# Kernel tuning notes

Hardware: AMD Instinct MI355X
Metric: run time of the kernel (lower is better)

## Reference

```python
import jax, jax.numpy as jnp
import numpy as np

TEMP = 5.0  # temperature_init
# All C(4,2)=6 keep-2-of-4 patterns for 2:4 semi-structured sparsity
PATTERNS = jnp.array([[1,1,0,0],[1,0,1,0],[1,0,0,1],[0,1,1,0],[0,1,0,1],[0,0,1,1]], dtype=jnp.float32)


def masked_linear(x, w, b, alpha, ids):
    # x: [N, I], w: [O, I], alpha: [A, O, I//4, 6], ids: [N]
    A, O, G, P = alpha.shape
    probs = jax.nn.softmax(alpha / TEMP, axis=-1)            # [A, O, G, 6]
    mask = jnp.einsum('aogp,pk->aogk', probs, PATTERNS)      # [A, O, G, 4]
    wm = w[None, :, :] * mask.reshape(A, O, G * 4)           # [A, O, I] per-agent masked weight
    y = jnp.einsum('ni,aoi->nao', x, wm)                     # dense per-agent GEMM
    y = jnp.take_along_axis(y, ids[:, None, None], axis=1)[:, 0, :]
    return y + b


def gru_cell(x, h, w_ih, w_hh, b_ih, b_hh):
    gi = x @ w_ih.T + b_ih
    gh = h @ w_hh.T + b_hh
    i_r, i_z, i_n = jnp.split(gi, 3, axis=-1)
    h_r, h_z, h_n = jnp.split(gh, 3, axis=-1)
    r = jax.nn.sigmoid(i_r + h_r)
    z = jax.nn.sigmoid(i_z + h_z)
    n = jnp.tanh(i_n + r * h_n)
    return (1.0 - z) * n + z * h


def setup_inputs() -> dict:
    key = jax.random.key(0)
    ks = jax.random.split(key, 20)
    B, A, E, H, NA = 1024, 8, 64, 512, 16
    s = 0.05
    d = {}
    d['inputs'] = jax.random.normal(ks[0], (B, A, E), jnp.float32)
    d['hidden_state'] = jax.random.normal(ks[1], (B, A, H), jnp.float32)
    d['agent_ids'] = jax.random.randint(ks[2], (B, A), 0, A, jnp.int32)
    d['fc1_w'] = jax.random.normal(ks[3], (H, E), jnp.float32) * s
    d['fc1_b'] = jax.random.normal(ks[4], (H,), jnp.float32) * s
    d['fc1_alpha'] = jax.random.normal(ks[5], (A, H, E // 4, 6), jnp.float32)
    d['gru_w_ih'] = jax.random.normal(ks[6], (3 * H, H), jnp.float32) * s
    d['gru_w_hh'] = jax.random.normal(ks[7], (3 * H, H), jnp.float32) * s
    d['gru_b_ih'] = jax.random.normal(ks[8], (3 * H,), jnp.float32) * s
    d['gru_b_hh'] = jax.random.normal(ks[9], (3 * H,), jnp.float32) * s
    d['fc2_w'] = jax.random.normal(ks[10], (H, H), jnp.float32) * s
    d['fc2_b'] = jax.random.normal(ks[11], (H,), jnp.float32) * s
    d['fc2_alpha'] = jax.random.normal(ks[12], (A, H, H // 4, 6), jnp.float32)
    d['fc3_w'] = jax.random.normal(ks[13], (H, H), jnp.float32) * s
    d['fc3_b'] = jax.random.normal(ks[14], (H,), jnp.float32) * s
    d['fc3_alpha'] = jax.random.normal(ks[15], (A, H, H // 4, 6), jnp.float32)
    d['fc4_w'] = jax.random.normal(ks[16], (NA, H), jnp.float32) * s
    d['fc4_b'] = jax.random.normal(ks[17], (NA,), jnp.float32) * s
    d['fc4_alpha'] = jax.random.normal(ks[18], (A, NA, H // 4, 6), jnp.float32)
    return d


def reference(inputs, hidden_state, agent_ids,
              fc1_w, fc1_b, fc1_alpha,
              gru_w_ih, gru_w_hh, gru_b_ih, gru_b_hh,
              fc2_w, fc2_b, fc2_alpha,
              fc3_w, fc3_b, fc3_alpha,
              fc4_w, fc4_b, fc4_alpha):
    b, a, e = inputs.shape
    H = hidden_state.shape[-1]
    x = inputs.reshape(-1, e)
    ids = agent_ids.reshape(-1)
    x = jax.nn.relu(masked_linear(x, fc1_w, fc1_b, fc1_alpha, ids))
    h = gru_cell(x, hidden_state.reshape(-1, H), gru_w_ih, gru_w_hh, gru_b_ih, gru_b_hh)
    q = jax.nn.relu(masked_linear(h, fc2_w, fc2_b, fc2_alpha, ids))
    q = jax.nn.relu(masked_linear(q, fc3_w, fc3_b, fc3_alpha, ids))
    q = masked_linear(q, fc4_w, fc4_b, fc4_alpha, ids)
    return q.reshape(b, a, -1), h.reshape(b, a, -1)
```

## Files before the change

### kernel.cpp

```cpp
#include <hip/hip_runtime.h>
#include <hip/hip_bf16.h>

typedef unsigned short ushort_t;
typedef __bf16 bf16x8 __attribute__((ext_vector_type(8)));
typedef unsigned short us8 __attribute__((ext_vector_type(8)));
typedef float f32x4 __attribute__((ext_vector_type(4)));

#define NPAD 8704
#define SENT (1 << 20)

__device__ __forceinline__ ushort_t f2b(float f) {
    union { float f; unsigned int u; } v; v.f = f;
    unsigned int u = v.u;
    unsigned int r = (u + 0x7FFFu + ((u >> 16) & 1u)) >> 16;
    return (ushort_t)r;
}
__device__ __forceinline__ float sigmoidf_(float x) {
    return 1.f / (1.f + __expf(-x));
}

__global__ void fill_kernel(float* out, long long n, float val) {
    long long i = (long long)blockIdx.x * blockDim.x + threadIdx.x;
    if (i < n) out[i] = val;
}

#define PACKSZ(O, K) ((long long)((O) >= 64 ? (O) >> 6 : 1) * ((K) >> 5) * 2048)

__global__ void sort_kernel(const int* __restrict__ ids, int N,
                            int* __restrict__ perm, int* __restrict__ seg,
                            int4* __restrict__ ttab, int* __restrict__ tcount) {
    __shared__ int hist[16][8];
    __shared__ int wbase[16][8];
    __shared__ int atot[8];
    __shared__ int abase[8];
    int tid = threadIdx.x, wave = tid >> 6, lane = tid & 63;
    int base = wave * 512;
    unsigned long long lt = (lane == 63) ? 0x7fffffffffffffffull
                                         : ((1ull << lane) - 1ull);
    int myid[8], rank[8];
    int run[8] = {0, 0, 0, 0, 0, 0, 0, 0};
    #pragma unroll
    for (int i = 0; i < 8; i++) myid[i] = ids[base + i * 64 + lane] & 7;
    #pragma unroll
    for (int i = 0; i < 8; i++) {
        int a = myid[i];
        int r = 0;
        #pragma unroll
        for (int a2 = 0; a2 < 8; a2++) {
            unsigned long long m = __ballot(a == a2);
            if (a2 == a) r = run[a2] + __popcll(m & lt);
            run[a2] += __popcll(m);
        }
        rank[i] = r;
    }
    if (lane == 0) {
        #pragma unroll
        for (int a = 0; a < 8; a++) hist[wave][a] = run[a];
    }
    __syncthreads();
    if (tid < 8) {
        int a = tid, s = 0;
        for (int w = 0; w < 16; w++) { wbase[w][a] = s; s += hist[w][a]; }
        atot[a] = s;
    }
    __syncthreads();
    if (tid == 0) {
        int s = 0;
        for (int a = 0; a < 8; a++) {
            abase[a] = s; seg[a] = s;
            s += (atot[a] + 63) & ~63;
        }
        seg[8] = s;
        int T = 0;
        for (int a = 0; a < 8; a++) {
            int e = abase[a] + atot[a];
            int pe = abase[a] + ((atot[a] + 63) & ~63);
            for (int m = abase[a]; m < pe; m += 64) {
                int z = e < m + 64 ? e : m + 64;
                ttab[T++] = make_int4(a, m, z, 0);
            }
        }
        *tcount = T;
    }
    __syncthreads();
    #pragma unroll
    for (int i = 0; i < 8; i++) {
        int a = myid[i];
        perm[abase[a] + wbase[wave][a] + rank[i]] = base + i * 64 + lane;
    }
    for (int a = 0; a < 8; a++) {
        int e = abase[a] + atot[a];
        int pe = abase[a] + ((atot[a] + 63) & ~63);
        for (int p2 = e + tid; p2 < pe; p2 += 1024) perm[p2] = SENT;
    }
    int Pend = abase[7] + ((atot[7] + 63) & ~63);
    for (int p2 = Pend + tid; p2 < NPAD; p2 += 1024) perm[p2] = SENT;
}

__device__ __forceinline__ void maskw_item(const float* __restrict__ alpha,
                                           const float* __restrict__ w,
                                           ushort_t* __restrict__ wm,
                                           long long idx, int O, int G, int dup) {
    int g = (int)(idx % G);
    long long t2 = idx / G;
    int o = (int)(t2 % O);
    int a = (int)(t2 / O);
    const float* al = alpha + idx * 6;
    float p[6];
    float mx = -1e30f;
    #pragma unroll
    for (int i = 0; i < 6; i++) { p[i] = al[i] * 0.2f; mx = fmaxf(mx, p[i]); }
    float s = 0.f;
    #pragma unroll
    for (int i = 0; i < 6; i++) { p[i] = __expf(p[i] - mx); s += p[i]; }
    float inv = 1.f / s;
    #pragma unroll
    for (int i = 0; i < 6; i++) p[i] *= inv;
    float mk[4] = { p[0] + p[1] + p[2], p[0] + p[3] + p[4],
                    p[1] + p[3] + p[5], p[2] + p[4] + p[5] };
    int K = G * 4;
    const float* wr = w + (long long)o * K + g * 4;
    ushort_t* base = wm + (long long)a * PACKSZ(O, K);
    int k0 = g * 4;
    int c = o >> 6, su = (o >> 4) & 3, n = o & 15;
    int kk = k0 >> 5, q = (k0 >> 3) & 3, e0 = k0 & 7;
    long long off = (((long long)(c * (K >> 5) + kk) * 4 + su) * 64 + (q * 16 + n)) * 8 + e0;
    #pragma unroll
    for (int t = 0; t < 4; t++) {
        ushort_t v = f2b(wr[t] * mk[t]);
        base[off + t] = v;
        if (dup) {
            base[off + t + 512] = v;
            base[off + t + 1024] = v;
            base[off + t + 1536] = v;
        }
    }
}

__device__ __forceinline__ void canon_gather_packed(const float* __restrict__ src,
                                                    ushort_t* __restrict__ dst,
                                                    const int* __restrict__ perm,
                                                    int ld, long long i) {
    int l = (int)(i & 63);
    int tt = (int)(i >> 6);
    int KK = ld >> 5;
    int mt = tt / KK, kk = tt - mt * KK;
    int row = perm[mt * 16 + (l & 15)];
    if (row >= 8192) row = 0;
    const float* s = src + (long long)row * ld + kk * 32 + (l >> 4) * 8;
    us8 v;
    #pragma unroll
    for (int e = 0; e < 8; e++) v[e] = f2b(s[e]);
    *(us8*)(dst + i * 8) = v;
}

__device__ __forceinline__ void canon_pack_item(const float* __restrict__ src,
                                                ushort_t* __restrict__ dst,
                                                long long i) {
    long long base = i * 8;
    int o_full = (int)(base >> 9);
    int k0 = (int)(base & 511);
    int g = o_full >> 9, o = o_full & 511;
    int c = o >> 6, su = (o >> 4) & 3, n = o & 15;
    int kk = k0 >> 5, q = (k0 >> 3) & 3;
    long long off = (long long)g * 262144 +
        (((long long)(c * 16 + kk) * 4 + su) * 64 + (q * 16 + n)) * 8;
    us8 v;
    #pragma unroll
    for (int e = 0; e < 8; e++) v[e] = f2b(src[base + e]);
    *(us8*)(dst + off) = v;
}

#define PB0 256
#define PB1 2048
#define PB2 2048
#define PB3 64
#define PB4 272
#define PB5 2176
#define PB6 384
#define PB7 384
#define PREP_BLOCKS (PB0+PB1+PB2+PB3+PB4+PB5+PB6+PB7)

__global__ void prep_kernel(const float* fc1_al, const float* fc1_w, ushort_t* wm1,
                            const float* fc2_al, const float* fc2_w, ushort_t* wm2,
                            const float* fc3_al, const float* fc3_w, ushort_t* wm3,
                            const float* fc4_al, const float* fc4_w, ushort_t* wm4,
                            const float* inputs, ushort_t* inp_pos,
                            const float* hidden, ushort_t* hid_pos,
                            const float* wih, ushort_t* wihp,
                            const float* whh, ushort_t* whhp,
                            const int* perm) {
    int b = blockIdx.x;
    int tid = threadIdx.x;
    if (b < PB0) { maskw_item(fc1_al, fc1_w, wm1, (long long)b * 256 + tid, 512, 16, 0); return; }
    b -= PB0;
    if (b < PB1) { maskw_item(fc2_al, fc2_w, wm2, (long long)b * 256 + tid, 512, 128, 0); return; }
    b -= PB1;
    if (b < PB2) { maskw_item(fc3_al, fc3_w, wm3, (long long)b * 256 + tid, 512, 128, 0); return; }
    b -= PB2;
    if (b < PB3) { maskw_item(fc4_al, fc4_w, wm4, (long long)b * 256 + tid, 16, 128, 1); return; }
    b -= PB3;
    if (b < PB4) { canon_gather_packed(inputs, inp_pos, perm, 64, (long long)b * 256 + tid); return; }
    b -= PB4;
    if (b < PB5) { canon_gather_packed(hidden, hid_pos, perm, 512, (long long)b * 256 + tid); return; }
    b -= PB5;
    if (b < PB6) { canon_pack_item(wih, wihp, (long long)b * 256 + tid); return; }
    b -= PB6;
    canon_pack_item(whh, whhp, (long long)b * 256 + tid);
}

template <typename OT, int NC, int PACKOUT>
__launch_bounds__(256, 4)
__global__ void gemm_tiled(const ushort_t* __restrict__ Apk, int K,
                           const ushort_t* __restrict__ Wpk, long long wstride,
                           const float* __restrict__ bias,
                           OT* __restrict__ Out, int ldo,
                           const int4* __restrict__ ttab,
                           const int* __restrict__ tcount,
                           const int* __restrict__ perm,
                           int O, int relu) {
    int t = blockIdx.x;
    if (t >= *tcount) return;
    int4 tt = ttab[t];
    int a = tt.x, pos0 = tt.y;
    constexpr int JJ = 2 * NC;

    int tid = threadIdx.x;
    int wave = tid >> 6, lane = tid & 63;
    int wr = (wave >> 1) & 1, wc = wave & 1;
    int quad = lane >> 4, l16 = lane & 15;

    int KK = K >> 5;
    int KKh = KK >> 1;
    int c_idx = blockIdx.y * NC + (NC == 2 ? wc : 0);
    const ushort_t* wb = Wpk + (long long)a * wstride +
        (long long)c_idx * KK * 2048 + lane * 8;
    const ushort_t* ap = Apk + (long long)(pos0 >> 4) * KK * 512 + lane * 8;

    f32x4 acc[2][JJ];
    #pragma unroll
    for (int i = 0; i < 2; i++)
        #pragma unroll
        for (int j = 0; j < JJ; j++) acc[i][j] = (f32x4){0.f, 0.f, 0.f, 0.f};

    bf16x8 aA[2], bA[JJ], aB[2], bB[JJ];

#define GLOADS(AR, BR, kkv) do {                                              \
    _Pragma("unroll") for (int i2 = 0; i2 < 2; i2++)                          \
        AR[i2] = *(const bf16x8*)(ap + ((long long)(wr * 2 + i2) * KK + (kkv)) * 512); \
    _Pragma("unroll") for (int j2 = 0; j2 < JJ; j2++) {                       \
        int su = (NC == 2) ? j2 : wc * 2 + j2;                                \
        BR[j2] = *(const bf16x8*)(wb + ((kkv) * 4 + su) * 512); }             \
} while (0)
#define GMFMAS(AR, BR) do {                                                   \
    _Pragma("unroll") for (int i2 = 0; i2 < 2; i2++)                          \
        _Pragma("unroll") for (int j2 = 0; j2 < JJ; j2++)                     \
            acc[i2][j2] = __builtin_amdgcn_mfma_f32_16x16x32_bf16(            \
                AR[i2], BR[j2], acc[i2][j2], 0, 0, 0);                        \
} while (0)

    GLOADS(aA, bA, 0);
    #pragma unroll 1
    for (int kk2 = 0; kk2 < KKh; kk2++) {
        GLOADS(aB, bB, kk2 * 2 + 1);
        GMFMAS(aA, bA);
        if (kk2 + 1 < KKh) GLOADS(aA, bA, kk2 * 2 + 2);
        GMFMAS(aB, bB);
    }
#undef GLOADS
#undef GMFMAS

    if constexpr (PACKOUT) {
        __shared__ ushort_t Cs[64 * 136];
        #pragma unroll
        for (int i = 0; i < 2; i++)
            #pragma unroll
            for (int j = 0; j < JJ; j++) {
                int colL = (NC == 2 ? wc * 64 : wc * 32) + j * 16 + l16;
                int col = blockIdx.y * (64 * NC) + colL;
                float bv = bias[col];
                #pragma unroll
                for (int r = 0; r < 4; r++) {
                    float v = acc[i][j][r] + bv;
                    if (relu) v = fmaxf(v, 0.f);
                    Cs[(wr * 32 + i * 16 + quad * 4 + r) * 136 + colL] = f2b(v);
                }
            }
        __syncthreads();
        int KKo = ldo >> 5;
        int kk0 = blockIdx.y * (2 * NC);
        constexpr int NKK = 2 * NC;
        #pragma unroll
        for (int s2 = 0; s2 < NKK; s2++) {
            int slot = s2 * 256 + tid;
            int l = slot & 63, t4 = slot >> 6;
            int mt = t4 / NKK, kkL = t4 - mt * NKK;
            us8 v = *(const us8*)(&Cs[(mt * 16 + (l & 15)) * 136 + kkL * 32 + (l >> 4) * 8]);
            *(us8*)((ushort_t*)Out + ((long long)((pos0 >> 4) + mt) * KKo + kk0 + kkL) * 512 + l * 8) = v;
        }
    } else {
        #pragma unroll
        for (int i = 0; i < 2; i++) {
            int mbase = wr * 32 + i * 16 + quad * 4;
            #pragma unroll
            for (int j = 0; j < JJ; j++) {
                int col = (NC == 2 ? wc * 64 : wc * 32) + j * 16 + l16;
                if (col < O) {
                    float bv = bias[col];
                    #pragma unroll
                    for (int r = 0; r < 4; r++) {
                        int pos = pos0 + mbase + r;
                        int orow = perm[pos];
                        if (orow < 8192) {
                            float v = acc[i][j][r] + bv;
                            if (relu) v = fmaxf(v, 0.f);
                            Out[(long long)orow * ldo + col] = v;
                        }
                    }
                }
            }
        }
    }
}

__launch_bounds__(256, 2)
__global__ void gru_fused(const ushort_t* __restrict__ y1,
                          const ushort_t* __restrict__ hid,
                          const float* __restrict__ hidden_f,
                          const ushort_t* __restrict__ wihp,
                          const ushort_t* __restrict__ whhp,
                          const float* __restrict__ bih,
                          const float* __restrict__ bhh,
                          const int* __restrict__ perm,
                          float* __restrict__ out_h_f,
                          ushort_t* __restrict__ hp,
                          const int4* __restrict__ ttab,
                          const int* __restrict__ tcount,
                          int H) {
    int t = blockIdx.x;
    if (t >= *tcount) return;
    int pos0 = ttab[t].y;
    int mt0 = pos0 >> 4;

    int tid = threadIdx.x;
    int wave = tid >> 6, lane = tid & 63;
    int wr = (wave >> 1) & 1, wc = wave & 1;
    int quad = lane >> 4, l16 = lane & 15;

    const ushort_t* ayp = y1 + (long long)mt0 * 16 * 512 + lane * 8;
    const ushort_t* ahp = hid + (long long)mt0 * 16 * 512 + lane * 8;

    long long cb = (long long)blockIdx.y * 16 * 2048 + lane * 8;
    const ushort_t* wbg[6];
    #pragma unroll
    for (int g = 0; g < 3; g++) wbg[g] = wihp + (long long)g * 262144 + cb;
    #pragma unroll
    for (int g = 3; g < 6; g++) wbg[g] = whhp + (long long)(g - 3) * 262144 + cb;

    f32x4 acc[4][2][2];
    #pragma unroll
    for (int g = 0; g < 4; g++)
        #pragma unroll
        for (int i = 0; i < 2; i++)
            #pragma unroll
            for (int j = 0; j < 2; j++) acc[g][i][j] = (f32x4){0.f, 0.f, 0.f, 0.f};

    bf16x8 ayA[2], ahA[2], bbA[6][2];
    bf16x8 ayB[2], ahB[2], bbB[6][2];

#define RLOADS(AY, AH, BB, kkv) do {                                          \
    _Pragma("unroll") for (int i2 = 0; i2 < 2; i2++) {                        \
        AY[i2] = *(const bf16x8*)(ayp + ((long long)(wr * 2 + i2) * 16 + (kkv)) * 512); \
        AH[i2] = *(const bf16x8*)(ahp + ((long long)(wr * 2 + i2) * 16 + (kkv)) * 512); } \
    _Pragma("unroll") for (int g2 = 0; g2 < 6; g2++)                          \
        _Pragma("unroll") for (int u2 = 0; u2 < 2; u2++)                      \
            BB[g2][u2] = *(const bf16x8*)(wbg[g2] + ((kkv) * 4 + wc * 2 + u2) * 512); \
} while (0)
#define RMFMAS(AY, AH, BB) do {                                               \
    _Pragma("unroll") for (int g2 = 0; g2 < 3; g2++) {                        \
        int ai = (g2 < 2) ? g2 : 2;                                           \
        int ah2 = (g2 < 2) ? g2 : 3;                                          \
        _Pragma("unroll") for (int i2 = 0; i2 < 2; i2++)                      \
            _Pragma("unroll") for (int j2 = 0; j2 < 2; j2++) {                \
                acc[ai][i2][j2] = __builtin_amdgcn_mfma_f32_16x16x32_bf16(    \
                    AY[i2], BB[g2][j2], acc[ai][i2][j2], 0, 0, 0);            \
                acc[ah2][i2][j2] = __builtin_amdgcn_mfma_f32_16x16x32_bf16(   \
                    AH[i2], BB[g2 + 3][j2], acc[ah2][i2][j2], 0, 0, 0); } }   \
} while (0)

    RLOADS(ayA, ahA, bbA, 0);
    #pragma unroll 1
    for (int kk2 = 0; kk2 < 8; kk2++) {
        RLOADS(ayB, ahB, bbB, kk2 * 2 + 1);
        RMFMAS(ayA, ahA, bbA);
        if (kk2 < 7) RLOADS(ayA, ahA, bbA, kk2 * 2 + 2);
        RMFMAS(ayB, ahB, bbB);
    }
#undef RLOADS
#undef RMFMAS

    __shared__ ushort_t Cs[64 * 72];
    int c0 = blockIdx.y * 64;
    #pragma unroll
    for (int i = 0; i < 2; i++) {
        #pragma unroll
        for (int r = 0; r < 4; r++) {
            int rowL = wr * 32 + i * 16 + quad * 4 + r;
            int pos = pos0 + rowL;
            int norig = perm[pos];
            bool realr = norig < 8192;
            int nr = realr ? norig : 0;
            #pragma unroll
            for (int j = 0; j < 2; j++) {
                int colL = wc * 32 + j * 16 + l16;
                int col = c0 + colL;
                float sr = acc[0][i][j][r] + bih[col] + bhh[col];
                float sz = acc[1][i][j][r] + bih[H + col] + bhh[H + col];
                float in_ = acc[2][i][j][r] + bih[2 * H + col];
                float hn = acc[3][i][j][r] + bhh[2 * H + col];
                float rg = sigmoidf_(sr);
                float zg = sigmoidf_(sz);
                float ng = tanhf(in_ + rg * hn);
                float hv = hidden_f[(long long)nr * H + col];
                float hnew = (1.f - zg) * ng + zg * hv;
                if (realr) out_h_f[(long long)norig * H + col] = hnew;
                Cs[rowL * 72 + colL] = f2b(hnew);
            }
        }
    }
    __syncthreads();
    #pragma unroll
    for (int s2 = 0; s2 < 2; s2++) {
        int slot = s2 * 256 + tid;
        int l = slot & 63, t4 = slot >> 6;
        int mt = t4 >> 1, kkL = t4 & 1;
        us8 v = *(const us8*)(&Cs[(mt * 16 + (l & 15)) * 72 + kkL * 32 + (l >> 4) * 8]);
        *(us8*)(hp + ((long long)(mt0 + mt) * 16 + blockIdx.y * 2 + kkL) * 512 + l * 8) = v;
    }
}

extern "C" void kernel_launch(void* const* d_in, const int* in_sizes, int n_in,
                              void* d_out, int out_size, void* d_ws, size_t ws_size,
                              hipStream_t stream) {
    (void)in_sizes; (void)n_in;
    const int N = 8192, A = 8, E = 64, H = 512, NA = 16;

    float* out_f = (float*)d_out;
    float* out_q = out_f;
    float* out_h = out_f + (size_t)N * NA;

    char* p = (char*)d_ws;
    auto alloc = [&](size_t b) { char* r = p; p += (b + 255) & ~(size_t)255; return r; };
    int*  perm   = (int*)alloc((size_t)NPAD * 4);
    int*  seg    = (int*)alloc(16 * 4);
    int4* ttab   = (int4*)alloc(144 * 16);
    int*  tcount = (int*)alloc(256);
    ushort_t* wm1     = (ushort_t*)alloc((size_t)A * PACKSZ(H, E) * 2);
    ushort_t* wm2     = (ushort_t*)alloc((size_t)A * PACKSZ(H, H) * 2);
    ushort_t* wm3     = (ushort_t*)alloc((size_t)A * PACKSZ(H, H) * 2);
    ushort_t* wm4     = (ushort_t*)alloc((size_t)A * PACKSZ(NA, H) * 2);
    ushort_t* y1      = (ushort_t*)alloc((size_t)NPAD * H * 2);
    ushort_t* inp_pos = (ushort_t*)alloc((size_t)NPAD * E * 2);
    ushort_t* hid_pos = (ushort_t*)alloc((size_t)NPAD * H * 2);
    ushort_t* wihp    = (ushort_t*)alloc((size_t)3 * H * H * 2);
    ushort_t* whhp    = (ushort_t*)alloc((size_t)3 * H * H * 2);
    ushort_t* hp      = (ushort_t*)alloc((size_t)NPAD * H * 2);
    size_t need = (size_t)(p - (char*)d_ws);
    ushort_t* q2 = y1;
    ushort_t* q3 = hid_pos;

    if (ws_size < need) {
        fill_kernel<<<(unsigned)((out_size + 255) / 256), 256, 0, stream>>>(
            out_f, out_size, 1000.f);
        return;
    }

    const float* inputs = (const float*)d_in[0];
    const float* hidden = (const float*)d_in[1];
    const int*   ids    = (const int*)d_in[2];
    const float* fc1_w  = (const float*)d_in[3];
    const float* fc1_b  = (const float*)d_in[4];
    const float* fc1_al = (const float*)d_in[5];
    const float* wih    = (const float*)d_in[6];
    const float* whh    = (const float*)d_in[7];
    const float* bih    = (const float*)d_in[8];
    const float* bhh    = (const float*)d_in[9];
    const float* fc2_w  = (const float*)d_in[10];
    const float* fc2_b  = (const float*)d_in[11];
    const float* fc2_al = (const float*)d_in[12];
    const float* fc3_w  = (const float*)d_in[13];
    const float* fc3_b  = (const float*)d_in[14];
    const float* fc3_al = (const float*)d_in[15];
    const float* fc4_w  = (const float*)d_in[16];
    const float* fc4_b  = (const float*)d_in[17];
    const float* fc4_al = (const float*)d_in[18];

    sort_kernel<<<1, 1024, 0, stream>>>(ids, N, perm, seg, ttab, tcount);

    prep_kernel<<<PREP_BLOCKS, 256, 0, stream>>>(
        fc1_al, fc1_w, wm1, fc2_al, fc2_w, wm2, fc3_al, fc3_w, wm3,
        fc4_al, fc4_w, wm4, inputs, inp_pos, hidden, hid_pos,
        wih, wihp, whh, whhp, perm);

    dim3 blk(256);
    gemm_tiled<ushort_t, 2, 1><<<dim3(136, H / 128), blk, 0, stream>>>(
        inp_pos, E, wm1, PACKSZ(H, E), fc1_b, y1, H, ttab, tcount,
        perm, H, 1);
    gru_fused<<<dim3(136, H / 64), blk, 0, stream>>>(
        y1, hid_pos, hidden, wihp, whhp, bih, bhh, perm, out_h, hp,
        ttab, tcount, H);
    gemm_tiled<ushort_t, 2, 1><<<dim3(136, H / 128), blk, 0, stream>>>(
        hp, H, wm2, PACKSZ(H, H), fc2_b, q2, H, ttab, tcount,
        perm, H, 1);
    gemm_tiled<ushort_t, 2, 1><<<dim3(136, H / 128), blk, 0, stream>>>(
        q2, H, wm3, PACKSZ(H, H), fc3_b, q3, H, ttab, tcount,
        perm, H, 1);
    gemm_tiled<float, 1, 0><<<dim3(136, 1), blk, 0, stream>>>(
        q3, H, wm4, PACKSZ(NA, H), fc4_b, out_q, NA, ttab, tcount,
        perm, NA, 0);
}
```

Baseline: 246.4 us.

## Stage GEMM and GRU operand tiles through LDS via direct global-to-LDS loads

Replaces the register double-buffered direct global loads in gemm_tiled and gru_fused with a double-buffered LDS staging scheme. Each wave issues global_load_lds for a share of the A and B chunks, and all waves then read their fragments from shared memory after a vmcnt wait and barrier. This removes duplicate global fetches of the same tiles by different waves and cuts VGPR pressure. In exchange it adds LDS traffic, a block-wide barrier on every k step, and lowers the occupancy hint from 4 to 3 blocks per CU.

```diff
diff --git a/kernel.cpp b/kernel.cpp
--- a/kernel.cpp
+++ b/kernel.cpp
@@ -17,6 +17,17 @@
 }
 __device__ __forceinline__ float sigmoidf_(float x) {
     return 1.f / (1.f + __expf(-x));
+}
+
+__device__ __forceinline__ void gl16(const ushort_t* g, ushort_t* l) {
+    __builtin_amdgcn_global_load_lds(
+        (const __attribute__((address_space(1))) unsigned int*)g,
+        (__attribute__((address_space(3))) unsigned int*)l, 16, 0, 0);
+}
+__device__ __forceinline__ void vm0_bar() {
+    asm volatile("s_waitcnt vmcnt(0)" ::: "memory");
+    __builtin_amdgcn_s_barrier();
+    __builtin_amdgcn_sched_barrier(0);
 }
 
 __global__ void fill_kernel(float* out, long long n, float val) {
@@ -210,7 +221,7 @@
 }
 
 template <typename OT, int NC, int PACKOUT>
-__launch_bounds__(256, 4)
+__launch_bounds__(256, 3)
 __global__ void gemm_tiled(const ushort_t* __restrict__ Apk, int K,
                            const ushort_t* __restrict__ Wpk, long long wstride,
                            const float* __restrict__ bias,
@@ -224,6 +235,11 @@
     int4 tt = ttab[t];
     int a = tt.x, pos0 = tt.y;
     constexpr int JJ = 2 * NC;
+    constexpr int NCH = 4 + 4 * NC;
+    constexpr int CPW = NCH / 4;
+
+    __shared__ ushort_t S[2][NCH * 512];
+    __shared__ ushort_t Cs[PACKOUT ? 64 * 136 : 2];
 
     int tid = threadIdx.x;
     int wave = tid >> 6, lane = tid & 63;
@@ -231,11 +247,27 @@
     int quad = lane >> 4, l16 = lane & 15;
 
     int KK = K >> 5;
-    int KKh = KK >> 1;
-    int c_idx = blockIdx.y * NC + (NC == 2 ? wc : 0);
-    const ushort_t* wb = Wpk + (long long)a * wstride +
-        (long long)c_idx * KK * 2048 + lane * 8;
-    const ushort_t* ap = Apk + (long long)(pos0 >> 4) * KK * 512 + lane * 8;
+
+    const ushort_t* cbase[CPW];
+    int cstep[CPW];
+    #pragma unroll
+    for (int q = 0; q < CPW; q++) {
+        int c = wave * CPW + q;
+        if (c < 4) {
+            cbase[q] = Apk + ((long long)((pos0 >> 4) + c) * KK) * 512 + lane * 8;
+            cstep[q] = 512;
+        } else {
+            int idx = c - 4, cblk = idx >> 2, su = idx & 3;
+            cbase[q] = Wpk + (long long)a * wstride +
+                (long long)(blockIdx.y * NC + cblk) * KK * 2048 + su * 512 + lane * 8;
+            cstep[q] = 2048;
+        }
+    }
+    auto STAGE = [&](int bufv, int kkv) {
+        #pragma unroll
+        for (int q = 0; q < CPW; q++)
+            gl16(cbase[q] + kkv * cstep[q], &S[bufv][(wave * CPW + q) * 512]);
+    };
 
     f32x4 acc[2][JJ];
     #pragma unroll
@@ -243,35 +275,31 @@
         #pragma unroll
         for (int j = 0; j < JJ; j++) acc[i][j] = (f32x4){0.f, 0.f, 0.f, 0.f};
 
-    bf16x8 aA[2], bA[JJ], aB[2], bB[JJ];
-
-#define GLOADS(AR, BR, kkv) do {                                              \
-    _Pragma("unroll") for (int i2 = 0; i2 < 2; i2++)                          \
-        AR[i2] = *(const bf16x8*)(ap + ((long long)(wr * 2 + i2) * KK + (kkv)) * 512); \
-    _Pragma("unroll") for (int j2 = 0; j2 < JJ; j2++) {                       \
-        int su = (NC == 2) ? j2 : wc * 2 + j2;                                \
-        BR[j2] = *(const bf16x8*)(wb + ((kkv) * 4 + su) * 512); }             \
-} while (0)
-#define GMFMAS(AR, BR) do {                                                   \
-    _Pragma("unroll") for (int i2 = 0; i2 < 2; i2++)                          \
-        _Pragma("unroll") for (int j2 = 0; j2 < JJ; j2++)                     \
-            acc[i2][j2] = __builtin_amdgcn_mfma_f32_16x16x32_bf16(            \
-                AR[i2], BR[j2], acc[i2][j2], 0, 0, 0);                        \
-} while (0)
-
-    GLOADS(aA, bA, 0);
-    #pragma unroll 1
-    for (int kk2 = 0; kk2 < KKh; kk2++) {
-        GLOADS(aB, bB, kk2 * 2 + 1);
-        GMFMAS(aA, bA);
-        if (kk2 + 1 < KKh) GLOADS(aA, bA, kk2 * 2 + 2);
-        GMFMAS(aB, bB);
-    }
-#undef GLOADS
-#undef GMFMAS
+    STAGE(0, 0);
+    vm0_bar();
+    int cur = 0;
+    for (int kk = 0; kk < KK; kk++) {
+        if (kk + 1 < KK) STAGE(cur ^ 1, kk + 1);
+        const ushort_t* Sc = S[cur];
+        bf16x8 af[2], bf[JJ];
+        #pragma unroll
+        for (int i = 0; i < 2; i++)
+            af[i] = *(const bf16x8*)(Sc + (wr * 2 + i) * 512 + lane * 8);
+        #pragma unroll
+        for (int j = 0; j < JJ; j++) {
+            int ch = (NC == 2) ? (4 + wc * 4 + j) : (4 + wc * 2 + j);
+            bf[j] = *(const bf16x8*)(Sc + ch * 512 + lane * 8);
+        }
+        #pragma unroll
+        for (int i = 0; i < 2; i++)
+            #pragma unroll
+            for (int j = 0; j < JJ; j++)
+                acc[i][j] = __builtin_amdgcn_mfma_f32_16x16x32_bf16(af[i], bf[j], acc[i][j], 0, 0, 0);
+        vm0_bar();
+        cur ^= 1;
+    }
 
     if constexpr (PACKOUT) {
-        __shared__ ushort_t Cs[64 * 136];
         #pragma unroll
         for (int i = 0; i < 2; i++)
             #pragma unroll
@@ -342,20 +370,37 @@
     int pos0 = ttab[t].y;
     int mt0 = pos0 >> 4;
 
+    __shared__ ushort_t S[2][32 * 512];
+    __shared__ ushort_t Cs[64 * 72];
+
     int tid = threadIdx.x;
     int wave = tid >> 6, lane = tid & 63;
     int wr = (wave >> 1) & 1, wc = wave & 1;
     int quad = lane >> 4, l16 = lane & 15;
 
-    const ushort_t* ayp = y1 + (long long)mt0 * 16 * 512 + lane * 8;
-    const ushort_t* ahp = hid + (long long)mt0 * 16 * 512 + lane * 8;
-
-    long long cb = (long long)blockIdx.y * 16 * 2048 + lane * 8;
-    const ushort_t* wbg[6];
-    #pragma unroll
-    for (int g = 0; g < 3; g++) wbg[g] = wihp + (long long)g * 262144 + cb;
-    #pragma unroll
-    for (int g = 3; g < 6; g++) wbg[g] = whhp + (long long)(g - 3) * 262144 + cb;
+    const ushort_t* cbase[8];
+    int cstep[8];
+    #pragma unroll
+    for (int q = 0; q < 8; q++) {
+        int c = wave * 8 + q;
+        if (c < 8) {
+            int mt = c & 3;
+            const ushort_t* srcp = (c < 4) ? y1 : hid;
+            cbase[q] = srcp + ((long long)(mt0 + mt) * 16) * 512 + lane * 8;
+            cstep[q] = 512;
+        } else {
+            int idx = c - 8, g = idx >> 2, su = idx & 3;
+            const ushort_t* gp = (g < 3) ? (wihp + (long long)g * 262144)
+                                         : (whhp + (long long)(g - 3) * 262144);
+            cbase[q] = gp + (long long)blockIdx.y * 16 * 2048 + su * 512 + lane * 8;
+            cstep[q] = 2048;
+        }
+    }
+    auto STAGE = [&](int bufv, int kkv) {
+        #pragma unroll
+        for (int q = 0; q < 8; q++)
+            gl16(cbase[q] + kkv * cstep[q], &S[bufv][(wave * 8 + q) * 512]);
+    };
 
     f32x4 acc[4][2][2];
     #pragma unroll
@@ -365,41 +410,43 @@
             #pragma unroll
             for (int j = 0; j < 2; j++) acc[g][i][j] = (f32x4){0.f, 0.f, 0.f, 0.f};
 
-    bf16x8 ayA[2], ahA[2], bbA[6][2];
-    bf16x8 ayB[2], ahB[2], bbB[6][2];
-
-#define RLOADS(AY, AH, BB, kkv) do {                                          \
-    _Pragma("unroll") for (int i2 = 0; i2 < 2; i2++) {                        \
-        AY[i2] = *(const bf16x8*)(ayp + ((long long)(wr * 2 + i2) * 16 + (kkv)) * 512); \
-        AH[i2] = *(const bf16x8*)(ahp + ((long long)(wr * 2 + i2) * 16 + (kkv)) * 512); } \
-    _Pragma("unroll") for (int g2 = 0; g2 < 6; g2++)                          \
-        _Pragma("unroll") for (int u2 = 0; u2 < 2; u2++)                      \
-            BB[g2][u2] = *(const bf16x8*)(wbg[g2] + ((kkv) * 4 + wc * 2 + u2) * 512); \
-} while (0)
-#define RMFMAS(AY, AH, BB) do {                                               \
-    _Pragma("unroll") for (int g2 = 0; g2 < 3; g2++) {                        \
-        int ai = (g2 < 2) ? g2 : 2;                                           \
-        int ah2 = (g2 < 2) ? g2 : 3;                                          \
-        _Pragma("unroll") for (int i2 = 0; i2 < 2; i2++)                      \
-            _Pragma("unroll") for (int j2 = 0; j2 < 2; j2++) {                \
-                acc[ai][i2][j2] = __builtin_amdgcn_mfma_f32_16x16x32_bf16(    \
-                    AY[i2], BB[g2][j2], acc[ai][i2][j2], 0, 0, 0);            \
-                acc[ah2][i2][j2] = __builtin_amdgcn_mfma_f32_16x16x32_bf16(   \
-                    AH[i2], BB[g2 + 3][j2], acc[ah2][i2][j2], 0, 0, 0); } }   \
-} while (0)
-
-    RLOADS(ayA, ahA, bbA, 0);
-    #pragma unroll 1
-    for (int kk2 = 0; kk2 < 8; kk2++) {
-        RLOADS(ayB, ahB, bbB, kk2 * 2 + 1);
-        RMFMAS(ayA, ahA, bbA);
-        if (kk2 < 7) RLOADS(ayA, ahA, bbA, kk2 * 2 + 2);
-        RMFMAS(ayB, ahB, bbB);
-    }
-#undef RLOADS
-#undef RMFMAS
-
-    __shared__ ushort_t Cs[64 * 72];
+    STAGE(0, 0);
+    vm0_bar();
+    int cur = 0;
+    for (int kk = 0; kk < 16; kk++) {
+        if (kk + 1 < 16) STAGE(cur ^ 1, kk + 1);
+        const ushort_t* Sc = S[cur];
+        bf16x8 ayf[2], ahf[2], bw[3][2], bu[3][2];
+        #pragma unroll
+        for (int u = 0; u < 2; u++) {
+            ayf[u] = *(const bf16x8*)(Sc + (wr * 2 + u) * 512 + lane * 8);
+            ahf[u] = *(const bf16x8*)(Sc + (4 + wr * 2 + u) * 512 + lane * 8);
+        }
+        #pragma unroll
+        for (int g = 0; g < 3; g++)
+            #pragma unroll
+            for (int u = 0; u < 2; u++) {
+                bw[g][u] = *(const bf16x8*)(Sc + (8 + g * 4 + wc * 2 + u) * 512 + lane * 8);
+                bu[g][u] = *(const bf16x8*)(Sc + (8 + (g + 3) * 4 + wc * 2 + u) * 512 + lane * 8);
+            }
+        #pragma unroll
+        for (int g = 0; g < 3; g++) {
+            int ai = (g < 2) ? g : 2;
+            int ah2 = (g < 2) ? g : 3;
+            #pragma unroll
+            for (int i = 0; i < 2; i++)
+                #pragma unroll
+                for (int j = 0; j < 2; j++) {
+                    acc[ai][i][j] = __builtin_amdgcn_mfma_f32_16x16x32_bf16(
+                        ayf[i], bw[g][j], acc[ai][i][j], 0, 0, 0);
+                    acc[ah2][i][j] = __builtin_amdgcn_mfma_f32_16x16x32_bf16(
+                        ahf[i], bu[g][j], acc[ah2][i][j], 0, 0, 0);
+                }
+        }
+        vm0_bar();
+        cur ^= 1;
+    }
+
     int c0 = blockIdx.y * 64;
     #pragma unroll
     for (int i = 0; i < 2; i++) {
```

New measurement: 255.8 us. 3.8% more time.
